# Optimization experiments

Hardware: AMD Instinct MI355X
Metric: run time of the kernel (lower is better)

## Reference

```python
import jax, jax.numpy as jnp
import numpy as np

WIN, DIL, PAD, H = 5, 1, 2, 8  # window, dilation, unfold padding, num_heads
C = 256
EPS = 1e-5

def _ln(z, g, b):
    m = jnp.mean(z, axis=-1, keepdims=True)
    v = jnp.mean((z - m) ** 2, axis=-1, keepdims=True)
    return (z - m) * jax.lax.rsqrt(v + EPS) * g + b

def setup_inputs() -> dict:
    key = jax.random.key(0)
    ks = jax.random.split(key, 16)
    s = 0.02
    d = {
        'x': jax.random.normal(ks[0], (32, C, 64, 25), jnp.float32),
        'ln1_g': jnp.ones((C,), jnp.float32), 'ln1_b': jnp.zeros((C,), jnp.float32),
        'q_w': jax.random.normal(ks[1], (C, C)) * s, 'q_b': jnp.zeros((C,)),
        'qa_w': jax.random.normal(ks[2], (C, H)) * s, 'qa_b': jnp.zeros((H,)),
        'k_w': jax.random.normal(ks[3], (C, C)) * s, 'k_b': jnp.zeros((C,)),
        'ka_w': jax.random.normal(ks[4], (C, H)) * s, 'ka_b': jnp.zeros((H,)),
        'v_w': jax.random.normal(ks[5], (C, C)) * s, 'v_b': jnp.zeros((C,)),
        't_w': jax.random.normal(ks[6], (C, C)) * s, 't_b': jnp.zeros((C,)),
        'p_w': jax.random.normal(ks[7], (C, C)) * s, 'p_b': jnp.zeros((C,)),
        'ffn_g': jnp.ones((C,)), 'ffn_b': jnp.zeros((C,)),
        'w1': jax.random.normal(ks[8], (C, C)) * s, 'b1': jnp.zeros((C,)),
        'w2': jax.random.normal(ks[9], (C, C)) * s, 'b2': jnp.zeros((C,)),
    }
    return d

def reference(x, ln1_g, ln1_b, q_w, q_b, qa_w, qa_b, k_w, k_b, ka_w, ka_b,
              v_w, v_b, t_w, t_b, p_w, p_b, ffn_g, ffn_b, w1, b1, w2, b2):
    N, Cc, T, V = x.shape
    hc = Cc // H
    scale = 1.0 / np.sqrt(hc)
    B, L = N * T, WIN * V
    xp = jnp.pad(x, ((0, 0), (0, 0), (PAD, PAD), (0, 0)))
    win = jnp.stack([xp[:, :, k * DIL:k * DIL + T, :] for k in range(WIN)], axis=2)  # (N,C,W,T,V)
    wx = win.transpose(0, 3, 2, 4, 1).reshape(B, L, Cc)
    nx = _ln(wx, ln1_g, ln1_b)
    # attention: softmax-pooled query
    q = nx @ q_w + q_b                                      # (B,L,C)
    qw = jax.nn.softmax(((q @ qa_w + qa_b) * scale).transpose(0, 2, 1), axis=-1)  # (B,H,L)
    qh = q.reshape(B, L, H, hc).transpose(0, 2, 1, 3)       # (B,H,L,hc)
    pq = jnp.einsum('bhl,bhld->bhd', qw, qh)                # (B,H,hc)
    k_ = nx @ k_w + k_b
    kq = k_ * pq.reshape(B, 1, Cc)
    kw = jax.nn.softmax(((kq @ ka_w + ka_b) * scale).transpose(0, 2, 1), axis=-1)
    kh = k_.reshape(B, L, H, hc).transpose(0, 2, 1, 3)
    pk = jnp.einsum('bhl,bhld->bhd', kw, kh)                # (B,H,hc)
    v_ = nx @ v_w + v_b
    vh = v_.reshape(B, L, H, hc).transpose(0, 2, 1, 3)
    kv = (vh * pk[:, :, None, :]).transpose(0, 2, 1, 3).reshape(B, L, Cc)
    kvh = (kv @ t_w + t_b).reshape(B, L, H, hc).transpose(0, 2, 1, 3)
    att = ((kvh + qh).transpose(0, 2, 1, 3).reshape(B, L, Cc)) @ p_w + p_b
    # average over window, residual with flattened x
    att = att.reshape(B, WIN, V, Cc).mean(axis=1)           # (B,V,C)
    att = att + x.transpose(0, 2, 3, 1).reshape(B, V, Cc)
    # FFN residual block
    f = _ln(att, ffn_g, ffn_b)
    f = jax.nn.gelu(f @ w1 + b1, approximate=False) @ w2 + b2
    y = f + att
    return y.reshape(N, T, V, Cc).transpose(0, 3, 1, 2)     # (N,C,T,V)
```

## Files before the change

kernel.cpp:

```cpp
#include <hip/hip_runtime.h>
#include <hip/hip_bf16.h>

typedef unsigned short u16b;
typedef __attribute__((ext_vector_type(8))) short short8;
typedef __attribute__((ext_vector_type(4))) float floatx4;

#define DEV static __device__ __forceinline__

DEV float sh2f(unsigned short s) { union { unsigned u; float f; } c; c.u = ((unsigned)s) << 16; return c.f; }
DEV unsigned short f2b(float f) {
    unsigned u = __float_as_uint(f);
    u += 0x7FFF + ((u >> 16) & 1);
    return (unsigned short)(u >> 16);
}

DEV void gload_lds16(const u16b* g, u16b* l) {
    __builtin_amdgcn_global_load_lds((const __attribute__((address_space(1))) void*)g,
                                     (__attribute__((address_space(3))) void*)l, 16, 0, 0);
}

constexpr int O_LN1G = 0, O_LN1B = 256, O_QB = 512, O_KB = 768, O_VB = 1024,
              O_TB = 1280, O_PB = 1536, O_FFNG = 1792, O_FFNB = 2048,
              O_B1 = 2304, O_B2 = 2560, O_QAB = 2816, O_KAB = 2824,
              O_QAW = 2832, O_KAW = 4880, O_CV = 6928;

__global__ void detect_k(const unsigned* __restrict__ xw, int* __restrict__ flag) {
    __shared__ int cnt;
    if (threadIdx.x == 0) cnt = 0;
    __syncthreads();
    int my = 0;
    for (int i = threadIdx.x; i < 4096; i += 256) {
        unsigned w = xw[i];
        unsigned e0 = (w >> 7) & 0xFFu;
        if (e0 >= 0xC0u) my++;
    }
    atomicAdd(&cnt, my);
    __syncthreads();
    if (threadIdx.x == 0) flag[0] = (cnt > 64) ? 1 : 0;
}

DEV unsigned short load_cvt(const void* src, size_t idx, int fp32) {
    return fp32 ? f2b(((const float*)src)[idx]) : ((const u16b*)src)[idx];
}

struct VecTab { const void* p[15]; int off[15]; int n[15]; };

__global__ __launch_bounds__(256)
void convert_vecs_k(VecTab tab, const int* __restrict__ flag, u16b* __restrict__ sv) {
    int e = blockIdx.x, fp32 = flag[0];
    const void* s = tab.p[e];
    int n = tab.n[e], off = tab.off[e];
    for (int i = threadIdx.x; i < n; i += 256)
        sv[off + i] = load_cvt(s, i, fp32);
}

struct W8 { const void* p[8]; unsigned dstoff[8]; unsigned rstride[8]; };

__global__ void wtrans_k(W8 tab, u16b* __restrict__ base, const int* __restrict__ flag) {
    __shared__ u16b tile[32][33];
    int fp32 = flag[0];
    const void* src = tab.p[blockIdx.z];
    u16b* dst = base + tab.dstoff[blockIdx.z];
    unsigned rs = tab.rstride[blockIdx.z];
    int c0 = blockIdx.x * 32, r0 = blockIdx.y * 32;
    int tx = threadIdx.x, ty = threadIdx.y;
#pragma unroll
    for (int i = 0; i < 32; i += 8)
        tile[ty + i][tx] = load_cvt(src, (size_t)(r0 + ty + i) * 256 + c0 + tx, fp32);
    __syncthreads();
#pragma unroll
    for (int i = 0; i < 32; i += 8)
        dst[(size_t)(c0 + ty + i) * rs + r0 + tx] = tile[tx][ty + i];
}

__global__ __launch_bounds__(256)
void transpose_in_k(const void* __restrict__ src, u16b* __restrict__ dst,
                    int rows, int cols, const int* __restrict__ flag) {
    __shared__ u16b tile[32][36];
    int fp32 = flag[0];
    int c0 = blockIdx.x * 32, r0 = blockIdx.y * 32;
    size_t zb = (size_t)blockIdx.z * rows * cols;
    int tid = threadIdx.x;
    int r = tid >> 3, c4 = (tid & 7) * 4;
    size_t sidx = zb + (size_t)(r0 + r) * cols + c0 + c4;
    if (fp32) {
        const float4 f4 = *(const float4*)((const float*)src + sidx);
        tile[r][c4]     = f2b(f4.x);
        tile[r][c4 + 1] = f2b(f4.y);
        tile[r][c4 + 2] = f2b(f4.z);
        tile[r][c4 + 3] = f2b(f4.w);
    } else {
        *(ushort4*)&tile[r][c4] = *(const ushort4*)((const u16b*)src + sidx);
    }
    __syncthreads();
    int c = tid >> 3, r4 = (tid & 7) * 4;
    ushort4 o;
    o.x = tile[r4][c]; o.y = tile[r4 + 1][c]; o.z = tile[r4 + 2][c]; o.w = tile[r4 + 3][c];
    *(ushort4*)&dst[zb + (size_t)(c0 + c) * rows + r0 + r4] = o;
}

__global__ __launch_bounds__(256)
void rowstats_k(const u16b* __restrict__ src, float2* __restrict__ st,
                int valid, int total) {
    int wv = threadIdx.x >> 6, lane = threadIdx.x & 63;
    int r = blockIdx.x * 4 + wv;
    if (r >= total) return;
    if (r >= valid) { if (lane == 0) st[r] = make_float2(0.f, 0.f); return; }
    int c = lane * 4;
    ushort4 raw = *(const ushort4*)&src[(size_t)r * 256 + c];
    float x0 = sh2f(raw.x), x1 = sh2f(raw.y), x2 = sh2f(raw.z), x3 = sh2f(raw.w);
    float s  = x0 + x1 + x2 + x3;
    float sq = x0 * x0 + x1 * x1 + x2 * x2 + x3 * x3;
#pragma unroll
    for (int o = 32; o; o >>= 1) { s += __shfl_xor(s, o); sq += __shfl_xor(sq, o); }
    float mean = s * (1.f / 256.f);
    float var  = sq * (1.f / 256.f) - mean * mean;
    if (lane == 0) st[r] = make_float2(mean, rsqrtf(var + 1e-5f));
}

__global__ __launch_bounds__(256)
void cvec_k(const u16b* __restrict__ pT, u16b* __restrict__ sv) {
    int j = threadIdx.x;
    float acc = sh2f(sv[O_PB + j]);
    const u16b* row = pT + (size_t)j * 256;
    for (int i = 0; i < 256; i += 8) {
        short8 t8 = *(const short8*)&sv[O_TB + i];
        short8 p8 = *(const short8*)&row[i];
#pragma unroll
        for (int u = 0; u < 8; ++u)
            acc += sh2f((unsigned short)t8[u]) * sh2f((unsigned short)p8[u]);
    }
    sv[O_CV + j] = f2b(acc);
}

template <int EPI, int LNA, int XY = 0, int STATS = 0>
__global__ __launch_bounds__(256, 4)
void gemm256(const u16b* __restrict__ A, int aStride, int K,
             const u16b* __restrict__ Wt,
             const u16b* __restrict__ bias, const u16b* __restrict__ addm,
             u16b* __restrict__ out, size_t osParam,
             const float2* __restrict__ stats, const float2* __restrict__ stats2,
             const u16b* __restrict__ gvec, const u16b* __restrict__ bvec,
             float2* __restrict__ statOut, const int* __restrict__ flag) {
    constexpr bool ALDS = (LNA == 0);
    __shared__ u16b As[64 * 72];
    __shared__ u16b Bs[128 * 64];
    __shared__ float sg[256], sb[256];
    __shared__ float2 spart[64][2];
    const int tid = threadIdx.x;
    const int m0 = (XY ? blockIdx.y : blockIdx.x) * 64;
    const int n0 = (XY ? blockIdx.x : blockIdx.y) * 128;
    const int wv = tid >> 6, lane = tid & 63;
    const int wrow = (wv >> 1) * 32, wcol = (wv & 1) * 64;
    const int fr = lane & 15;
    const int fq = lane >> 4;
    floatx4 acc[2][4];
    const floatx4 zero = {0.f, 0.f, 0.f, 0.f};
#pragma unroll
    for (int i = 0; i < 2; ++i)
#pragma unroll
        for (int j = 0; j < 4; ++j) acc[i][j] = zero;

    float2 strow[2];
    if (LNA) {
        sg[tid] = sh2f(gvec[tid]);
        sb[tid] = sh2f(bvec[tid]);
#pragma unroll
        for (int kk = 0; kk < 2; ++kk) {
            int r = m0 + (tid >> 3) + kk * 32;
            if (LNA == 2) {
                float2 a = stats[r], b = stats2[r];
                float mean = (a.x + b.x) * (1.f / 256.f);
                float var  = (a.y + b.y) * (1.f / 256.f) - mean * mean;
                strow[kk] = make_float2(mean, rsqrtf(var + 1e-5f));
            } else {
                strow[kk] = stats[r];
            }
        }
        __syncthreads();
    }

    for (int kt = 0; kt < K; kt += 64) {
        if (ALDS) {
#pragma unroll
            for (int kk = 0; kk < 2; ++kk) {
                int chunk = tid + kk * 256;
                int row = chunk >> 3, col = (chunk & 7) * 8;
                int scol = col ^ ((row & 7) << 3);
                gload_lds16(&A[(size_t)(m0 + row) * aStride + kt + scol], &As[chunk * 8]);
            }
        } else {
#pragma unroll
            for (int kk = 0; kk < 2; ++kk) {
                int chunk = tid + kk * 256;
                int row = chunk >> 3, col = (chunk & 7) * 8;
                union { uint4 u; unsigned short h[8]; } rw;
                rw.u = *(const uint4*)&A[(size_t)(m0 + row) * aStride + kt + col];
#pragma unroll
                for (int j = 0; j < 8; ++j) {
                    float f = sh2f(rw.h[j]);
                    f = (f - strow[kk].x) * strow[kk].y * sg[kt + col + j] + sb[kt + col + j];
                    rw.h[j] = f2b(f);
                }
                *(uint4*)&As[row * 72 + col] = rw.u;
            }
        }
#pragma unroll
        for (int kk = 0; kk < 4; ++kk) {
            int chunk = tid + kk * 256;
            int row = chunk >> 3, col = (chunk & 7) * 8;
            int scol = col ^ ((row & 7) << 3);
            gload_lds16(&Wt[(size_t)(n0 + row) * K + kt + scol], &Bs[chunk * 8]);
        }
        __syncthreads();
#pragma unroll
        for (int s = 0; s < 2; ++s) {
            short8 af[2], bfr[4];
#pragma unroll
            for (int i = 0; i < 2; ++i) {
                int ar = wrow + i * 16 + fr;
                if (ALDS)
                    af[i] = *(const short8*)((const char*)As +
                              ((ar * 128 + s * 64 + fq * 16) ^ ((ar & 7) << 4)));
                else
                    af[i] = *(short8*)&As[ar * 72 + s * 32 + fq * 8];
            }
#pragma unroll
            for (int j = 0; j < 4; ++j) {
                int br = wcol + j * 16 + fr;
                bfr[j] = *(const short8*)((const char*)Bs +
                          ((br * 128 + s * 64 + fq * 16) ^ ((br & 7) << 4)));
            }
#pragma unroll
            for (int i = 0; i < 2; ++i)
#pragma unroll
                for (int j = 0; j < 4; ++j)
                    acc[i][j] = __builtin_amdgcn_mfma_f32_16x16x32_bf16(af[i], bfr[j], acc[i][j], 0, 0, 0);
        }
        __syncthreads();
    }
    float bv[4];
#pragma unroll
    for (int j = 0; j < 4; ++j) bv[j] = bias ? sh2f(bias[n0 + wcol + j * 16 + fr]) : 0.f;

    if (EPI == 5) {
        int fp32o = flag[0];
#pragma unroll
        for (int i = 0; i < 2; ++i) {
            int row0 = m0 + wrow + i * 16 + fq * 4;
            int n = row0 / 1600;
            int tv = row0 - n * 1600;
#pragma unroll
            for (int j = 0; j < 4; ++j) {
                int col = n0 + wcol + j * 16 + fr;
                float v4[4];
#pragma unroll
                for (int r = 0; r < 4; ++r)
                    v4[r] = acc[i][j][r] + bv[j] + sh2f(addm[(size_t)(row0 + r) * 256 + col]);
                size_t oidx = ((size_t)n * 256 + col) * 1600 + tv;
                if (fp32o) {
                    float4 o = {v4[0], v4[1], v4[2], v4[3]};
                    *(float4*)((float*)out + oidx) = o;
                } else {
                    ushort4 o;
                    o.x = f2b(v4[0]); o.y = f2b(v4[1]); o.z = f2b(v4[2]); o.w = f2b(v4[3]);
                    *(ushort4*)&out[oidx] = o;
                }
            }
        }
    } else {
#pragma unroll
        for (int i = 0; i < 2; ++i) {
#pragma unroll
            for (int r = 0; r < 4; ++r) {
                int row = m0 + wrow + i * 16 + fq * 4 + r;
                size_t ro = (size_t)row * 256;
                float s1 = 0.f, s2 = 0.f;
#pragma unroll
                for (int j = 0; j < 4; ++j) {
                    int col = n0 + wcol + j * 16 + fr;
                    float val = acc[i][j][r] + bv[j];
                    if (EPI == 2) val += sh2f(addm[ro + col]);
                    if (EPI == 3) val = 0.5f * val * (1.0f + erff(val * 0.70710678118654752f));
                    if (STATS) { s1 += val; s2 += val * val; }
                    if (EPI == 4)      out[(size_t)(col >> 8) * osParam + ro + (col & 255)] = f2b(val);
                    else if (EPI == 0) out[(size_t)row * osParam + col] = f2b(val);
                    else               out[ro + col] = f2b(val);
                }
                if (STATS) {
#pragma unroll
                    for (int mm = 1; mm < 16; mm <<= 1) {
                        s1 += __shfl_xor(s1, mm);
                        s2 += __shfl_xor(s2, mm);
                    }
                    if (fr == 0) spart[wrow + i * 16 + fq * 4 + r][wv & 1] = make_float2(s1, s2);
                }
            }
        }
        if (STATS) {
            __syncthreads();
            if (tid < 64) {
                float2 a = spart[tid][0], b = spart[tid][1];
                statOut[(size_t)(n0 >> 7) * 51200 + m0 + tid] = make_float2(a.x + b.x, a.y + b.y);
            }
        }
    }
}


DEV void logits_union(const u16b* __restrict__ S, const u16b* su, const int* srow,
                      float* slog, const u16b* __restrict__ sv, int aboff, int tid) {
    int wv = tid >> 6, lane = tid & 63;
    int fr = lane & 15, fq = lane >> 4;
    float abv = sh2f(sv[aboff + (fr & 7)]);
    for (int f = wv; f < 10; f += 8) {
        floatx4 acc = {0.f, 0.f, 0.f, 0.f};
        const u16b* Ar = S + (size_t)srow[f * 16 + fr] * 256;
#pragma unroll
        for (int s = 0; s < 8; ++s) {
            short8 a  = *(const short8*)&Ar[s * 32 + fq * 8];
            short8 bb = *(const short8*)&su[fr * 260 + s * 32 + fq * 8];
            acc = __builtin_amdgcn_mfma_f32_16x16x32_bf16(a, bb, acc, 0, 0, 0);
        }
#pragma unroll
        for (int r = 0; r < 4; ++r)
            slog[(f * 16 + fq * 4 + r) * 18 + fr] = (acc[r] + abv) * 0.17677669529663687f;
    }
}

template <int KC>
DEV void softmax16(const float* slog, float* wqA, float* wqB, int tid) {
    int wv = tid >> 6, lane = tid & 63;
#pragma unroll
    for (int c = 0; c < 2; ++c) {
        int combo = wv + c * 8;
        int dt = combo >> 3, h = combo & 7;
        int col = KC ? combo : h;
        const float* src = slog + (size_t)(dt * 25) * 18 + col;
        float v0 = (lane < 125) ? src[lane * 18] : -1e30f;
        float v1 = (lane + 64 < 125) ? src[(lane + 64) * 18] : -1e30f;
        float mx = fmaxf(v0, v1);
#pragma unroll
        for (int o = 32; o; o >>= 1) mx = fmaxf(mx, __shfl_xor(mx, o));
        float e0 = (lane < 125) ? __expf(v0 - mx) : 0.f;
        float e1 = (lane + 64 < 125) ? __expf(v1 - mx) : 0.f;
        float s = e0 + e1;
#pragma unroll
        for (int o = 32; o; o >>= 1) s += __shfl_xor(s, o);
        float inv = 1.f / s;
        float* dst = dt ? wqB : wqA;
        int off = dt ? 25 : 0;
        if (lane < 125) dst[(lane + off) * 9 + h] = e0 * inv;
        if (lane + 64 < 125) dst[(lane + 64 + off) * 9 + h] = e1 * inv;
    }
}

DEV void pool_union(const u16b* __restrict__ S, const int* srow,
                    const float* wqA, const float* wqB, float* scratch,
                    float* out0, float* out1, int tid) {
    int c8 = (tid & 31) * 8, h = c8 >> 5, ls = tid >> 5;
    float a0[8] = {0.f,0.f,0.f,0.f,0.f,0.f,0.f,0.f};
    float a1[8] = {0.f,0.f,0.f,0.f,0.f,0.f,0.f,0.f};
    for (int u = ls; u < 150; u += 16) {
        float w0 = wqA[u * 9 + h];
        float w1 = wqB[u * 9 + h];
        short8 d8 = *(const short8*)&S[(size_t)srow[u] * 256 + c8];
#pragma unroll
        for (int j = 0; j < 8; ++j) {
            float f = sh2f((unsigned short)d8[j]);
            a0[j] += w0 * f;
            a1[j] += w1 * f;
        }
    }
#pragma unroll
    for (int j = 0; j < 8; ++j) {
        a0[j] += __shfl_xor(a0[j], 32);
        a1[j] += __shfl_xor(a1[j], 32);
    }
    int wv = tid >> 6, lane = tid & 63;
    if (lane < 32) {
#pragma unroll
        for (int j = 0; j < 8; ++j) scratch[wv * 260 + c8 + j] = a0[j];
    }
    __syncthreads();
    if (tid < 256) {
        float s = 0.f;
#pragma unroll
        for (int q = 0; q < 8; ++q) s += scratch[q * 260 + tid];
        out0[tid] = s;
    }
    __syncthreads();
    if (lane < 32) {
#pragma unroll
        for (int j = 0; j < 8; ++j) scratch[wv * 260 + c8 + j] = a1[j];
    }
    __syncthreads();
    if (tid < 256) {
        float s = 0.f;
#pragma unroll
        for (int q = 0; q < 8; ++q) s += scratch[q * 260 + tid];
        out1[tid] = s;
    }
    __syncthreads();
}

DEV void wmean2(const u16b* __restrict__ S, const int* srow,
                const float* scale0, const float* scale1,
                u16b* __restrict__ CB, int base, int nb, int tid) {
    for (int i = tid; i < 800; i += 512) {
        int v = i >> 5, c8 = (i & 31) * 8;
        float s0[8] = {0.f,0.f,0.f,0.f,0.f,0.f,0.f,0.f};
        float s1[8] = {0.f,0.f,0.f,0.f,0.f,0.f,0.f,0.f};
#pragma unroll
        for (int w = 0; w < 6; ++w) {
            short8 d8 = *(const short8*)&S[(size_t)srow[w * 25 + v] * 256 + c8];
#pragma unroll
            for (int j = 0; j < 8; ++j) {
                float f = sh2f((unsigned short)d8[j]);
                if (w < 5)  s0[j] += f;
                if (w >= 1) s1[j] += f;
            }
        }
        unsigned short o0[8], o1[8];
#pragma unroll
        for (int j = 0; j < 8; ++j) {
            float m0 = s0[j] * 0.2f, m1 = s1[j] * 0.2f;
            if (scale0) { m0 *= scale0[c8 + j]; m1 *= scale1[c8 + j]; }
            o0[j] = f2b(m0); o1[j] = f2b(m1);
        }
        *(uint4*)&CB[((size_t)nb * 25 + v) * 512 + base + c8]       = *(uint4*)o0;
        *(uint4*)&CB[((size_t)(nb + 1) * 25 + v) * 512 + base + c8] = *(uint4*)o1;
    }
}

__global__ __launch_bounds__(512)
void pool_fused2(const u16b* __restrict__ qf, const u16b* __restrict__ kf,
                 const u16b* __restrict__ vf, const u16b* __restrict__ sv,
                 u16b* __restrict__ CB) {
    __shared__ int srow[160];
    __shared__ u16b su[16 * 260];
    __shared__ float slog[160 * 18];
    __shared__ float wqA[160 * 9], wqB[160 * 9];
    __shared__ float spq[2][256], spk[2][256];
    int bid = blockIdx.x;
    int b2 = ((bid & 7) << 7) | (bid >> 3);
    int n = b2 >> 5, t0 = (b2 & 31) * 2;
    int nb = n * 64 + t0;
    int tid = threadIdx.x;
    if (tid < 160) {
        int u = tid < 150 ? tid : 149;
        int tl = u / 25, v = u - tl * 25, tt = t0 + tl - 2;
        srow[tid] = ((unsigned)tt < 64u) ? (n * 64 + tt) * 25 + v : 51200;
    }
    for (int i = tid; i < 2048; i += 512) {
        int c = i >> 3, h = i & 7;
        su[h * 260 + c] = sv[O_QAW + i];
    }
    for (int i = tid; i < 1440; i += 512) { wqA[i] = 0.f; wqB[i] = 0.f; }
    __syncthreads();

    logits_union(qf, su, srow, slog, sv, O_QAB, tid);
    __syncthreads();
    softmax16<0>(slog, wqA, wqB, tid);
    __syncthreads();

    pool_union(qf, srow, wqA, wqB, slog, spq[0], spq[1], tid);

    wmean2(qf, srow, nullptr, nullptr, CB, 256, nb, tid);

    for (int i = tid; i < 4096; i += 512) {
        int c = i >> 4, h16 = i & 15;
        float w = sh2f(sv[O_KAW + c * 8 + (h16 & 7)]) * spq[h16 >> 3][c];
        su[h16 * 260 + c] = f2b(w);
    }
    for (int i = tid; i < 1440; i += 512) { wqA[i] = 0.f; wqB[i] = 0.f; }
    __syncthreads();

    logits_union(kf, su, srow, slog, sv, O_KAB, tid);
    __syncthreads();
    softmax16<1>(slog, wqA, wqB, tid);
    __syncthreads();

    pool_union(kf, srow, wqA, wqB, slog, spk[0], spk[1], tid);

    wmean2(vf, srow, spk[0], spk[1], CB, 0, nb, tid);
}

extern "C" void kernel_launch(void* const* d_in, const int* in_sizes, int n_in,
                              void* d_out, int out_size, void* d_ws, size_t ws_size,
                              hipStream_t stream) {
    (void)in_sizes; (void)n_in; (void)out_size; (void)ws_size;
    const void* x    = d_in[0];
    const void* ln1g = d_in[1];  const void* ln1b = d_in[2];
    const void* q_w  = d_in[3];  const void* q_b  = d_in[4];
    const void* qa_w = d_in[5];  const void* qa_b = d_in[6];
    const void* k_w  = d_in[7];  const void* k_b  = d_in[8];
    const void* ka_w = d_in[9];  const void* ka_b = d_in[10];
    const void* v_w  = d_in[11]; const void* v_b  = d_in[12];
    const void* t_w  = d_in[13]; const void* t_b  = d_in[14];
    const void* p_w  = d_in[15]; const void* p_b  = d_in[16];
    const void* ffng = d_in[17]; const void* ffnb = d_in[18];
    const void* w1   = d_in[19]; const void* b1   = d_in[20];
    const void* w2   = d_in[21]; const void* b2   = d_in[22];

    char* ws = (char*)d_ws;
    size_t off = 0;
    auto alloc = [&](size_t bytes) { void* p = ws + off; off += (bytes + 255) & ~(size_t)255; return p; };
    const size_t RPAD = 51328;
    int*    flag = (int*)alloc(256);
    u16b*   sv   = (u16b*)alloc(8192 * 2);
    u16b*   wT   = (u16b*)alloc((size_t)7 * 65536 * 2);
    u16b*   cW   = (u16b*)alloc((size_t)256 * 512 * 2);
    u16b*   xT   = (u16b*)alloc(RPAD * 256 * 2);
    u16b*   Bq   = (u16b*)alloc(RPAD * 256 * 2);
    u16b*   Bk   = (u16b*)alloc(RPAD * 256 * 2);
    u16b*   Bv   = (u16b*)alloc(RPAD * 256 * 2);
    u16b*   CB   = (u16b*)alloc((size_t)51200 * 512 * 2);
    u16b*   att  = (u16b*)alloc((size_t)51200 * 256 * 2);
    float2* st1  = (float2*)alloc(RPAD * 8);
    float2* st2p = (float2*)alloc((size_t)2 * 51200 * 8);

    u16b* pT  = wT + 3 * 65536;
    u16b* tT  = wT + 4 * 65536;
    u16b* w1T = wT + 5 * 65536;
    u16b* w2T = wT + 6 * 65536;

    detect_k<<<1, 256, 0, stream>>>((const unsigned*)x, flag);
    VecTab tab;
    const void* vp[15] = {ln1g, ln1b, q_b, k_b, v_b, t_b, p_b, ffng, ffnb, b1, b2, qa_b, ka_b, qa_w, ka_w};
    const int vo[15] = {O_LN1G, O_LN1B, O_QB, O_KB, O_VB, O_TB, O_PB, O_FFNG, O_FFNB, O_B1, O_B2, O_QAB, O_KAB, O_QAW, O_KAW};
    const int vn[15] = {256, 256, 256, 256, 256, 256, 256, 256, 256, 256, 256, 8, 8, 2048, 2048};
    for (int i = 0; i < 15; ++i) { tab.p[i] = vp[i]; tab.off[i] = vo[i]; tab.n[i] = vn[i]; }
    convert_vecs_k<<<15, 256, 0, stream>>>(tab, flag, sv);

    dim3 tb(32, 8);
    W8 wt;
    const void* wsrc[8] = {q_w, k_w, v_w, p_w, t_w, w1, w2, p_w};
    for (int i = 0; i < 8; ++i) {
        wt.p[i] = wsrc[i];
        wt.dstoff[i] = (i < 7) ? (unsigned)(i * 65536) : (unsigned)((cW + 256) - wT);
        wt.rstride[i] = (i < 7) ? 256u : 512u;
    }
    wtrans_k<<<dim3(8, 8, 8), tb, 0, stream>>>(wt, wT, flag);
    cvec_k<<<1, 256, 0, stream>>>(pT, sv);
    gemm256<0, 0><<<dim3(4, 2), 256, 0, stream>>>(pT, 256, 256, tT, nullptr, nullptr,
                                                  cW, 512, nullptr, nullptr, nullptr, nullptr,
                                                  nullptr, nullptr);
    transpose_in_k<<<dim3(50, 8, 32), 256, 0, stream>>>(x, xT, 256, 1600, flag);
    rowstats_k<<<12832, 256, 0, stream>>>(xT, st1, 51200, 51328);
    gemm256<4, 1, 1><<<dim3(6, 802), 256, 0, stream>>>(xT, 256, 256, wT, sv + O_QB, nullptr,
                                                       Bq, RPAD * 256, st1, nullptr,
                                                       sv + O_LN1G, sv + O_LN1B, nullptr, nullptr);
    pool_fused2<<<1024, 512, 0, stream>>>(Bq, Bk, Bv, sv, CB);
    gemm256<2, 0, 1, 1><<<dim3(2, 800), 256, 0, stream>>>(CB, 512, 512, cW, sv + O_CV, xT,
                                                          att, 256, nullptr, nullptr,
                                                          nullptr, nullptr, st2p, nullptr);
    gemm256<3, 2, 1><<<dim3(2, 800), 256, 0, stream>>>(att, 256, 256, w1T, sv + O_B1, nullptr,
                                                       Bq, 256, st2p, st2p + 51200,
                                                       sv + O_FFNG, sv + O_FFNB, nullptr, nullptr);
    gemm256<5, 0, 1><<<dim3(2, 800), 256, 0, stream>>>(Bq, 256, 256, w2T, sv + O_B2, att,
                                                       (u16b*)d_out, 0, nullptr, nullptr,
                                                       nullptr, nullptr, nullptr, flag);
}
```

Before: 373.0 us.

## Stage GEMM epilogues through LDS for coalesced 16-byte stores and pad shared arrays

The GEMM epilogues now write accumulator tiles into shared memory reusing the B-tile buffer. They then read them back so each thread issues 16-byte coalesced global stores, and the residual-add loads are vectorised as well. The transposed EPI 5 path stages the residual matrix through LDS, and the EPI 2 path computes LN statistics from the staged rows. The pooling kernel's logits and scratch strides are padded to cut LDS bank conflicts and to use float4 writes. In exchange this adds extra syncthreads, enlarges the shared buffer, and writes per-16-lane stats directly to global memory.

```diff
diff --git a/kernel.cpp b/kernel.cpp
--- a/kernel.cpp
+++ b/kernel.cpp
@@ -144,9 +144,8 @@
              float2* __restrict__ statOut, const int* __restrict__ flag) {
     constexpr bool ALDS = (LNA == 0);
     __shared__ u16b As[64 * 72];
-    __shared__ u16b Bs[128 * 64];
+    __shared__ u16b Bs[8448];
     __shared__ float sg[256], sb[256];
-    __shared__ float2 spart[64][2];
     const int tid = threadIdx.x;
     const int m0 = (XY ? blockIdx.y : blockIdx.x) * 64;
     const int n0 = (XY ? blockIdx.x : blockIdx.y) * 128;
@@ -244,19 +243,29 @@
     for (int j = 0; j < 4; ++j) bv[j] = bias ? sh2f(bias[n0 + wcol + j * 16 + fr]) : 0.f;
 
     if (EPI == 5) {
+        u16b* CT = Bs;
+#pragma unroll
+        for (int kk = 0; kk < 4; ++kk) {
+            int chunk = tid + kk * 256;
+            int row = chunk >> 4, c8 = (chunk & 15) * 8;
+            *(uint4*)&CT[row * 132 + c8] = *(const uint4*)&addm[(size_t)(m0 + row) * 256 + n0 + c8];
+        }
+        __syncthreads();
         int fp32o = flag[0];
 #pragma unroll
         for (int i = 0; i < 2; ++i) {
-            int row0 = m0 + wrow + i * 16 + fq * 4;
+            int lr0 = wrow + i * 16 + fq * 4;
+            int row0 = m0 + lr0;
             int n = row0 / 1600;
             int tv = row0 - n * 1600;
 #pragma unroll
             for (int j = 0; j < 4; ++j) {
-                int col = n0 + wcol + j * 16 + fr;
+                int lc = wcol + j * 16 + fr;
+                int col = n0 + lc;
                 float v4[4];
 #pragma unroll
                 for (int r = 0; r < 4; ++r)
-                    v4[r] = acc[i][j][r] + bv[j] + sh2f(addm[(size_t)(row0 + r) * 256 + col]);
+                    v4[r] = acc[i][j][r] + bv[j] + sh2f(CT[(lr0 + r) * 132 + lc]);
                 size_t oidx = ((size_t)n * 256 + col) * 1600 + tv;
                 if (fp32o) {
                     float4 o = {v4[0], v4[1], v4[2], v4[3]};
@@ -268,24 +277,35 @@
                 }
             }
         }
-    } else {
-#pragma unroll
-        for (int i = 0; i < 2; ++i) {
-#pragma unroll
-            for (int r = 0; r < 4; ++r) {
-                int row = m0 + wrow + i * 16 + fq * 4 + r;
-                size_t ro = (size_t)row * 256;
+    } else if (EPI == 2) {
+        float* CTf = (float*)Bs;
+#pragma unroll
+        for (int half = 0; half < 2; ++half) {
+            if ((wrow >> 5) == half) {
+#pragma unroll
+                for (int i = 0; i < 2; ++i)
+#pragma unroll
+                    for (int r = 0; r < 4; ++r) {
+                        int lrow = i * 16 + fq * 4 + r;
+#pragma unroll
+                        for (int j = 0; j < 4; ++j)
+                            CTf[lrow * 132 + wcol + j * 16 + fr] = acc[i][j][r] + bv[j];
+                    }
+            }
+            __syncthreads();
+#pragma unroll
+            for (int kk = 0; kk < 2; ++kk) {
+                int chunk = tid + kk * 256;
+                int row = chunk >> 4, c8 = (chunk & 15) * 8;
+                int grow = m0 + half * 32 + row, gcol = n0 + c8;
+                union { uint4 u; unsigned short h[8]; } am, ow;
+                am.u = *(const uint4*)&addm[(size_t)grow * 256 + gcol];
                 float s1 = 0.f, s2 = 0.f;
 #pragma unroll
-                for (int j = 0; j < 4; ++j) {
-                    int col = n0 + wcol + j * 16 + fr;
-                    float val = acc[i][j][r] + bv[j];
-                    if (EPI == 2) val += sh2f(addm[ro + col]);
-                    if (EPI == 3) val = 0.5f * val * (1.0f + erff(val * 0.70710678118654752f));
-                    if (STATS) { s1 += val; s2 += val * val; }
-                    if (EPI == 4)      out[(size_t)(col >> 8) * osParam + ro + (col & 255)] = f2b(val);
-                    else if (EPI == 0) out[(size_t)row * osParam + col] = f2b(val);
-                    else               out[ro + col] = f2b(val);
+                for (int u8 = 0; u8 < 8; ++u8) {
+                    float v = CTf[row * 132 + c8 + u8] + sh2f(am.h[u8]);
+                    s1 += v; s2 += v * v;
+                    ow.h[u8] = f2b(v);
                 }
                 if (STATS) {
 #pragma unroll
@@ -293,16 +313,36 @@
                         s1 += __shfl_xor(s1, mm);
                         s2 += __shfl_xor(s2, mm);
                     }
-                    if (fr == 0) spart[wrow + i * 16 + fq * 4 + r][wv & 1] = make_float2(s1, s2);
+                    if ((tid & 15) == 0)
+                        statOut[(size_t)(n0 >> 7) * 51200 + grow] = make_float2(s1, s2);
                 }
-            }
-        }
-        if (STATS) {
+                *(uint4*)&out[(size_t)grow * 256 + gcol] = ow.u;
+            }
             __syncthreads();
-            if (tid < 64) {
-                float2 a = spart[tid][0], b = spart[tid][1];
-                statOut[(size_t)(n0 >> 7) * 51200 + m0 + tid] = make_float2(a.x + b.x, a.y + b.y);
-            }
+        }
+    } else {
+        u16b* CT = Bs;
+#pragma unroll
+        for (int i = 0; i < 2; ++i)
+#pragma unroll
+            for (int r = 0; r < 4; ++r) {
+                int lrow = wrow + i * 16 + fq * 4 + r;
+#pragma unroll
+                for (int j = 0; j < 4; ++j) {
+                    float val = acc[i][j][r] + bv[j];
+                    if (EPI == 3) val = 0.5f * val * (1.0f + erff(val * 0.70710678118654752f));
+                    CT[lrow * 132 + wcol + j * 16 + fr] = f2b(val);
+                }
+            }
+        __syncthreads();
+#pragma unroll
+        for (int kk = 0; kk < 4; ++kk) {
+            int chunk = tid + kk * 256;
+            int row = chunk >> 4, c8 = (chunk & 15) * 8;
+            int grow = m0 + row, gcol = n0 + c8;
+            uint4 cw = *(const uint4*)&CT[row * 132 + c8];
+            if (EPI == 4)      *(uint4*)&out[(size_t)(gcol >> 8) * osParam + (size_t)grow * 256 + (gcol & 255)] = cw;
+            else               *(uint4*)&out[(size_t)grow * osParam + gcol] = cw;
         }
     }
 }
@@ -324,7 +364,7 @@
         }
 #pragma unroll
         for (int r = 0; r < 4; ++r)
-            slog[(f * 16 + fq * 4 + r) * 18 + fr] = (acc[r] + abv) * 0.17677669529663687f;
+            slog[(f * 16 + fq * 4 + r) * 19 + fr] = (acc[r] + abv) * 0.17677669529663687f;
     }
 }
 
@@ -336,9 +376,9 @@
         int combo = wv + c * 8;
         int dt = combo >> 3, h = combo & 7;
         int col = KC ? combo : h;
-        const float* src = slog + (size_t)(dt * 25) * 18 + col;
-        float v0 = (lane < 125) ? src[lane * 18] : -1e30f;
-        float v1 = (lane + 64 < 125) ? src[(lane + 64) * 18] : -1e30f;
+        const float* src = slog + (size_t)(dt * 25) * 19 + col;
+        float v0 = (lane < 125) ? src[lane * 19] : -1e30f;
+        float v1 = (lane + 64 < 125) ? src[(lane + 64) * 19] : -1e30f;
         float mx = fmaxf(v0, v1);
 #pragma unroll
         for (int o = 32; o; o >>= 1) mx = fmaxf(mx, __shfl_xor(mx, o));
@@ -379,26 +419,28 @@
     }
     int wv = tid >> 6, lane = tid & 63;
     if (lane < 32) {
-#pragma unroll
-        for (int j = 0; j < 8; ++j) scratch[wv * 260 + c8 + j] = a0[j];
+        float4 lo = {a0[0], a0[1], a0[2], a0[3]}, hi = {a0[4], a0[5], a0[6], a0[7]};
+        *(float4*)&scratch[wv * 264 + c8]     = lo;
+        *(float4*)&scratch[wv * 264 + c8 + 4] = hi;
     }
     __syncthreads();
     if (tid < 256) {
         float s = 0.f;
 #pragma unroll
-        for (int q = 0; q < 8; ++q) s += scratch[q * 260 + tid];
+        for (int q = 0; q < 8; ++q) s += scratch[q * 264 + tid];
         out0[tid] = s;
     }
     __syncthreads();
     if (lane < 32) {
-#pragma unroll
-        for (int j = 0; j < 8; ++j) scratch[wv * 260 + c8 + j] = a1[j];
+        float4 lo = {a1[0], a1[1], a1[2], a1[3]}, hi = {a1[4], a1[5], a1[6], a1[7]};
+        *(float4*)&scratch[wv * 264 + c8]     = lo;
+        *(float4*)&scratch[wv * 264 + c8 + 4] = hi;
     }
     __syncthreads();
     if (tid < 256) {
         float s = 0.f;
 #pragma unroll
-        for (int q = 0; q < 8; ++q) s += scratch[q * 260 + tid];
+        for (int q = 0; q < 8; ++q) s += scratch[q * 264 + tid];
         out1[tid] = s;
     }
     __syncthreads();
@@ -439,7 +481,7 @@
                  u16b* __restrict__ CB) {
     __shared__ int srow[160];
     __shared__ u16b su[16 * 260];
-    __shared__ float slog[160 * 18];
+    __shared__ float slog[160 * 19];
     __shared__ float wqA[160 * 9], wqB[160 * 9];
     __shared__ float spq[2][256], spk[2][256];
     int bid = blockIdx.x;
```

After: 369.6 us. About the same (-0.9%).
